# Kernel tuning notes

Measured on AMD Instinct MI355X. Metric: run time of the kernel, lower is better.

Reference implementation:

```python
import jax, jax.numpy as jnp
import numpy as np

B, N, A, M, H, KD, VD, O = 256, 2048, 256, 256, 8, 32, 32, 256
EPS = 1e-10

def setup_inputs() -> dict:
    key = jax.random.key(0)
    ks = jax.random.split(key, 8)
    return {
        "q_data": jax.random.normal(ks[0], (B, N, A), dtype=jnp.float32),
        "m_data": jax.random.normal(ks[1], (B, N, M), dtype=jnp.float32),
        "q_mask": jnp.ones((B, N, 1), dtype=jnp.float32),
        "bias": jnp.zeros((B, 1, N), dtype=jnp.float32),
        "query_w": 0.02 * jax.random.normal(ks[2], (A, H, KD), dtype=jnp.float32),
        "key_w": 0.02 * jax.random.normal(ks[3], (M, KD), dtype=jnp.float32),
        "value_w": 0.02 * jax.random.normal(ks[4], (M, VD), dtype=jnp.float32),
        "gating_w": 0.02 * jax.random.normal(ks[5], (A, H, VD), dtype=jnp.float32),
        "gating_b": jnp.zeros((H, VD), dtype=jnp.float32),
        "output_w": 0.02 * jax.random.normal(ks[6], (H, VD, O), dtype=jnp.float32),
        "output_b": jnp.zeros((O,), dtype=jnp.float32),
    }

def reference(q_data, m_data, q_mask, bias, query_w, key_w, value_w,
              gating_w, gating_b, output_w, output_b):
    # masked mean over the query axis: q_mask [B,N,1] broadcasts over channels
    q_avg = jnp.sum(q_mask * q_data, axis=1) / (jnp.sum(q_mask, axis=1) + EPS)  # [B,A]
    kd = query_w.shape[-1]
    q = jnp.einsum('ba,ahc->bhc', q_avg, query_w) * kd ** (-0.5)  # [B,H,KD]
    k = jnp.einsum('bka,ac->bkc', m_data, key_w)                  # [B,N,KD]
    v = jnp.einsum('bka,ac->bkc', m_data, value_w)                # [B,N,VD]
    # the incoming `bias` arg is overwritten by the module, as in the original
    attn_bias = 1e9 * (q_mask[:, None, :, 0] - 1.0)               # [B,1,N]
    logits = jnp.einsum('bhc,bkc->bhk', q, k) + attn_bias         # [B,H,N]
    weights = jax.nn.softmax(logits, axis=-1)
    weighted_avg = jnp.einsum('bhk,bkc->bhc', weights, v)         # [B,H,VD]
    # gating == True
    gate = jax.nn.sigmoid(jnp.einsum('bqc,chv->bqhv', q_data, gating_w) + gating_b)
    gated = weighted_avg[:, None] * gate                          # [B,N,H,VD]
    out = jnp.einsum('bqhc,hco->bqo', gated, output_w) + output_b # [B,N,O]
    return out
```

## Files before the change

### kernel.cpp

```cpp
#include <hip/hip_runtime.h>

#define B_ 256
#define N_ 2048
#define A_ 256
#define M_ 256
#define H_ 8
#define KD_ 32
#define VD_ 32
#define O_ 256

typedef float f32x4 __attribute__((ext_vector_type(4)));
typedef __bf16 bf16x8 __attribute__((ext_vector_type(8)));
typedef unsigned short u16x8 __attribute__((ext_vector_type(8)));

union FragU { u16x8 u; bf16x8 b; };

__device__ __forceinline__ unsigned short f2bf(float f) {
  union { __bf16 b; unsigned short u; } c;
  c.b = (__bf16)f;
  return c.u;
}
__device__ __forceinline__ float bf2f(unsigned short h) {
  return __uint_as_float(((unsigned int)h) << 16);
}

__device__ __forceinline__ void gll16(const void* gsrc, void* ldst) {
  __builtin_amdgcn_global_load_lds(
      (const __attribute__((address_space(1))) void*)gsrc,
      (__attribute__((address_space(3))) void*)ldst, 16, 0, 0);
}

__global__ void pack_weights(const float* __restrict__ gating_w,
                             const float* __restrict__ output_w,
                             const float* __restrict__ key_w,
                             const float* __restrict__ value_w,
                             unsigned short* __restrict__ wg,
                             unsigned short* __restrict__ wo,
                             unsigned short* __restrict__ wkv) {
  int idx = blockIdx.x * 256 + threadIdx.x;
  int j = idx & 7;
  int lane = (idx >> 3) & 63;
  int rest = idx >> 9;
  int kc = rest & 7, ct = rest >> 3;
  int row = kc * 32 + ((lane >> 4) << 3) + j;
  int col = ct * 16 + (lane & 15);
  wg[idx] = f2bf(gating_w[row * 256 + col]);
  wo[idx] = f2bf(output_w[row * 256 + col]);
  if (idx < 16384) {
    float v = (col < 32) ? key_w[row * 32 + col] : value_w[row * 32 + (col - 32)];
    wkv[idx] = f2bf(v);
  }
}

__global__ void reduce_q(const float* __restrict__ qd, const float* __restrict__ qm,
                         const float* __restrict__ qw, float* __restrict__ q_out) {
  int b = blockIdx.x;
  int t = threadIdx.x;
  int l = t & 63, g = t >> 6;
  const float* qdb = qd + (size_t)b * N_ * A_;
  const float* qmb = qm + (size_t)b * N_;
  f32x4 sum = {0.f, 0.f, 0.f, 0.f};
  float msum = 0.f;
  for (int n = g; n < N_; n += 16) {
    float m = qmb[n];
    msum += m;
    f32x4 v = *(const f32x4*)(qdb + (size_t)n * A_ + l * 4);
    sum += m * v;
  }
  __shared__ float s[16][256];
  __shared__ float ms[16];
  __shared__ float qavg[256];
  *(f32x4*)&s[g][l * 4] = sum;
  if (l == 0) ms[g] = msum;
  __syncthreads();
  if (t < 256) {
    float tot = 0.f;
#pragma unroll
    for (int k = 0; k < 16; k++) tot += s[k][t];
    float mt = 0.f;
#pragma unroll
    for (int k = 0; k < 16; k++) mt += ms[k];
    qavg[t] = tot / (mt + 1e-10f);
  }
  __syncthreads();
  if (t < 256) {
    float acc = 0.f;
    for (int a2 = 0; a2 < 256; a2++) acc += qavg[a2] * qw[a2 * 256 + t];
    q_out[b * 256 + t] = acc * 0.17677669529663687f;
  }
}

__global__ void kv_gemm(const float* __restrict__ md,
                        const unsigned short* __restrict__ wkv,
                        unsigned short* __restrict__ kv) {
  int t = threadIdx.x;
  int w = t >> 6, l = t & 63, q = l >> 4, l15 = l & 15;
  size_t r0 = (size_t)blockIdx.x * 128;
  f32x4 acc[2][4] = {};
  for (int kc = 0; kc < 8; kc++) {
    FragU bfr[4];
#pragma unroll
    for (int ct = 0; ct < 4; ct++)
      bfr[ct].u = *(const u16x8*)(wkv + (((ct * 8 + kc) * 64 + l) << 3));
    FragU af[2];
#pragma unroll
    for (int rt = 0; rt < 2; rt++) {
      size_t row = r0 + (size_t)(w * 32 + rt * 16 + l15);
      const float4* s4 = (const float4*)(md + row * 256 + kc * 32 + q * 8);
      float4 u0 = s4[0], u1 = s4[1];
      af[rt].u = (u16x8){f2bf(u0.x), f2bf(u0.y), f2bf(u0.z), f2bf(u0.w),
                         f2bf(u1.x), f2bf(u1.y), f2bf(u1.z), f2bf(u1.w)};
    }
#pragma unroll
    for (int ct = 0; ct < 4; ct++) {
      acc[0][ct] = __builtin_amdgcn_mfma_f32_16x16x32_bf16(af[0].b, bfr[ct].b, acc[0][ct], 0, 0, 0);
      acc[1][ct] = __builtin_amdgcn_mfma_f32_16x16x32_bf16(af[1].b, bfr[ct].b, acc[1][ct], 0, 0, 0);
    }
  }
#pragma unroll
  for (int rt = 0; rt < 2; rt++)
#pragma unroll
    for (int ct = 0; ct < 4; ct++)
#pragma unroll
      for (int r = 0; r < 4; r++) {
        size_t row = r0 + (size_t)(w * 32 + rt * 16 + q * 4 + r);
        kv[row * 64 + ct * 16 + l15] = f2bf(acc[rt][ct][r]);
      }
}

__global__ void attn_softmax(const unsigned short* __restrict__ kv,
                             const float* __restrict__ qv,
                             const float* __restrict__ qm,
                             float* __restrict__ wa) {
  int b = blockIdx.x, t = threadIdx.x;
  __shared__ float lg[8][2048];
  __shared__ float red[4][256];
  __shared__ float inv_s[8];
  const float* qb = qv + b * 256;
  const float* qmb = qm + (size_t)b * N_;
  for (int n = t; n < N_; n += 1024) {
    const u16x8* kr = (const u16x8*)(kv + ((size_t)(b * N_ + n)) * 64);
    float kf[32];
#pragma unroll
    for (int c8 = 0; c8 < 4; c8++) {
      u16x8 kk = kr[c8];
#pragma unroll
      for (int j = 0; j < 8; j++) kf[c8 * 8 + j] = bf2f(kk[j]);
    }
    float bias_n = 1e9f * (qmb[n] - 1.0f);
#pragma unroll
    for (int h = 0; h < 8; h++) {
      float d = 0.f;
#pragma unroll
      for (int c = 0; c < 32; c++) d += qb[h * 32 + c] * kf[c];
      lg[h][n] = d + bias_n;
    }
  }
  __syncthreads();
  if (t < 256) {
    int h = t >> 5, i = t & 31;
    float m = -3.0e38f;
    for (int n = i; n < N_; n += 32) m = fmaxf(m, lg[h][n]);
#pragma unroll
    for (int off = 16; off; off >>= 1) m = fmaxf(m, __shfl_xor(m, off));
    float s = 0.f;
    for (int n = i; n < N_; n += 32) {
      float e = __expf(lg[h][n] - m);
      lg[h][n] = e;
      s += e;
    }
#pragma unroll
    for (int off = 16; off; off >>= 1) s += __shfl_xor(s, off);
    if (i == 0) inv_s[h] = 1.0f / s;
  }
  __syncthreads();
  {
    int c = t & 31, h = (t >> 5) & 7, nq = t >> 8;
    const unsigned short* vb = kv + ((size_t)b * N_ + nq * 512) * 64 + 32 + c;
    const float* lgh = &lg[h][nq * 512];
    float acc = 0.f;
#pragma unroll 8
    for (int n = 0; n < 512; n++) acc += lgh[n] * bf2f(vb[(size_t)n * 64]);
    red[nq][t & 255] = acc;
  }
  __syncthreads();
  if (t < 256) {
    float r = red[0][t] + red[1][t] + red[2][t] + red[3][t];
    wa[b * 256 + t] = r * inv_s[t >> 5];
  }
}

__launch_bounds__(256)
__global__ void gate_out(const float* __restrict__ qd,
                         const unsigned short* __restrict__ wg,
                         const unsigned short* __restrict__ wo,
                         const float* __restrict__ wa,
                         const float* __restrict__ gb,
                         const float* __restrict__ ob,
                         float* __restrict__ out) {
  int blk = blockIdx.x;
  int b = blk >> 5, tile = blk & 31;
  int t = threadIdx.x;
  int w = t >> 6, l = t & 63, q = l >> 4, l15 = l & 15;
  __shared__ __attribute__((aligned(16))) unsigned short wst[2][16384];
  __shared__ __attribute__((aligned(16))) unsigned short Pt[4][16][40];
  __shared__ float wa_s[256], gb_s[256], ob_s[256];
  wa_s[t] = wa[b * 256 + t];
  gb_s[t] = gb[t];
  ob_s[t] = ob[t];
  size_t rowbase = (size_t)b * N_ + tile * 64;

  {
    const char* wgb = (const char*)wg;
    const char* wob = (const char*)wo;
    char* dst = (char*)&wst[0][0];
#pragma unroll
    for (int i = 0; i < 4; i++) {
      int ch = i * 4 + w;
      gll16(wgb + ch * 1024 + l * 16, dst + ch * 1024);
      gll16(wob + ch * 8192 + l * 16, dst + 16384 + ch * 1024);
    }
  }

  FragU af[8];
  {
    const float* src = qd + (rowbase + (size_t)(w * 16 + l15)) * 256 + q * 8;
#pragma unroll
    for (int kc = 0; kc < 8; kc++) {
      float4 u0 = *(const float4*)(src + kc * 32);
      float4 u1 = *(const float4*)(src + kc * 32 + 4);
      af[kc].u = (u16x8){f2bf(u0.x), f2bf(u0.y), f2bf(u0.z), f2bf(u0.w),
                         f2bf(u1.x), f2bf(u1.y), f2bf(u1.z), f2bf(u1.w)};
    }
  }
  f32x4 acc[16] = {};
  __syncthreads();

  for (int g = 0; g < 8; g++) {
    int cur = g & 1;
    if (g < 7) {
      const char* wgb = (const char*)wg + (size_t)(g + 1) * 16384;
      const char* wob = (const char*)wo + (size_t)(g + 1) * 1024;
      char* dst = (char*)&wst[cur ^ 1][0];
#pragma unroll
      for (int i = 0; i < 4; i++) {
        int ch = i * 4 + w;
        gll16(wgb + ch * 1024 + l * 16, dst + ch * 1024);
        gll16(wob + ch * 8192 + l * 16, dst + 16384 + ch * 1024);
      }
    }
    const unsigned short* wsl = &wst[cur][0];
    f32x4 gacc[2] = {};
#pragma unroll
    for (int kc = 0; kc < 8; kc++) {
      FragU b0, b1;
      b0.u = *(const u16x8*)(wsl + ((0 * 8 + kc) * 64 + l) * 8);
      b1.u = *(const u16x8*)(wsl + ((1 * 8 + kc) * 64 + l) * 8);
      gacc[0] = __builtin_amdgcn_mfma_f32_16x16x32_bf16(af[kc].b, b0.b, gacc[0], 0, 0, 0);
      gacc[1] = __builtin_amdgcn_mfma_f32_16x16x32_bf16(af[kc].b, b1.b, gacc[1], 0, 0, 0);
    }
#pragma unroll
    for (int ctl = 0; ctl < 2; ctl++) {
      int colg = ctl * 16 + l15;
      int col = g * 32 + colg;
      float wav = wa_s[col], gbv = gb_s[col];
#pragma unroll
      for (int r = 0; r < 4; r++) {
        float x = gacc[ctl][r] + gbv;
        float gate = 1.0f / (1.0f + __expf(-x));
        Pt[w][q * 4 + r][colg] = f2bf(wav * gate);
      }
    }
    FragU pf;
    pf.u = *(const u16x8*)&Pt[w][l15][q * 8];
#pragma unroll
    for (int ct = 0; ct < 16; ct++) {
      FragU bo;
      bo.u = *(const u16x8*)(wsl + 8192 + (ct * 64 + l) * 8);
      acc[ct] = __builtin_amdgcn_mfma_f32_16x16x32_bf16(pf.b, bo.b, acc[ct], 0, 0, 0);
    }
    __syncthreads();
  }
#pragma unroll
  for (int ct = 0; ct < 16; ct++) {
    int col = ct * 16 + l15;
    float obv = ob_s[col];
    size_t orow = (rowbase + (size_t)(w * 16 + q * 4)) * 256 + col;
#pragma unroll
    for (int r = 0; r < 4; r++)
      out[orow + (size_t)r * 256] = acc[ct][r] + obv;
  }
}

extern "C" void kernel_launch(void* const* d_in, const int* in_sizes, int n_in,
                              void* d_out, int out_size, void* d_ws, size_t ws_size,
                              hipStream_t stream) {
  const float* q_data   = (const float*)d_in[0];
  const float* m_data   = (const float*)d_in[1];
  const float* q_mask   = (const float*)d_in[2];
  const float* query_w  = (const float*)d_in[4];
  const float* key_w    = (const float*)d_in[5];
  const float* value_w  = (const float*)d_in[6];
  const float* gating_w = (const float*)d_in[7];
  const float* gating_b = (const float*)d_in[8];
  const float* output_w = (const float*)d_in[9];
  const float* output_b = (const float*)d_in[10];
  float* out = (float*)d_out;

  char* ws = (char*)d_ws;
  float* q_ws            = (float*)(ws);
  float* wa_ws           = (float*)(ws + (256 << 10));
  unsigned short* wg_ws  = (unsigned short*)(ws + (512 << 10));
  unsigned short* wo_ws  = (unsigned short*)(ws + (640 << 10));
  unsigned short* wkv_ws = (unsigned short*)(ws + (768 << 10));
  unsigned short* kv_ws  = (unsigned short*)(ws + (800 << 10));

  pack_weights<<<256, 256, 0, stream>>>(gating_w, output_w, key_w, value_w,
                                        wg_ws, wo_ws, wkv_ws);
  reduce_q<<<B_, 1024, 0, stream>>>(q_data, q_mask, query_w, q_ws);
  kv_gemm<<<(B_ * N_) / 128, 256, 0, stream>>>(m_data, wkv_ws, kv_ws);
  attn_softmax<<<B_, 1024, 0, stream>>>(kv_ws, q_ws, q_mask, wa_ws);
  gate_out<<<(B_ * N_) / 64, 256, 0, stream>>>(q_data, wg_ws, wo_ws, wa_ws,
                                               gating_b, output_b, out);
}
```

Before: 1.513 ms.

## Replace double-buffered weight staging with split single buffers to raise occupancy

Drops the double-buffered 64KB weight staging in gate_out in favour of two single 16KB buffers, one for gating weights and one for output weights. Each buffer's next slice is loaded right after its last use, with an extra barrier per iteration, so the gating-weight load overlaps the output MFMAs. Launch bounds now request 4 blocks per SM. The goal is higher occupancy to hide latency, at the cost of less prefetch distance and more synchronisation.

```diff
diff --git a/kernel.cpp b/kernel.cpp
--- a/kernel.cpp
+++ b/kernel.cpp
@@ -190,7 +190,7 @@
   }
 }
 
-__launch_bounds__(256)
+__launch_bounds__(256, 4)
 __global__ void gate_out(const float* __restrict__ qd,
                          const unsigned short* __restrict__ wg,
                          const unsigned short* __restrict__ wo,
@@ -202,7 +202,8 @@
   int b = blk >> 5, tile = blk & 31;
   int t = threadIdx.x;
   int w = t >> 6, l = t & 63, q = l >> 4, l15 = l & 15;
-  __shared__ __attribute__((aligned(16))) unsigned short wst[2][16384];
+  __shared__ __attribute__((aligned(16))) unsigned short wsg[8192];
+  __shared__ __attribute__((aligned(16))) unsigned short wso[8192];
   __shared__ __attribute__((aligned(16))) unsigned short Pt[4][16][40];
   __shared__ float wa_s[256], gb_s[256], ob_s[256];
   wa_s[t] = wa[b * 256 + t];
@@ -213,12 +214,11 @@
   {
     const char* wgb = (const char*)wg;
     const char* wob = (const char*)wo;
-    char* dst = (char*)&wst[0][0];
 #pragma unroll
     for (int i = 0; i < 4; i++) {
       int ch = i * 4 + w;
-      gll16(wgb + ch * 1024 + l * 16, dst + ch * 1024);
-      gll16(wob + ch * 8192 + l * 16, dst + 16384 + ch * 1024);
+      gll16(wgb + ch * 1024 + l * 16, (char*)wsg + ch * 1024);
+      gll16(wob + ch * 8192 + l * 16, (char*)wso + ch * 1024);
     }
   }
 
@@ -237,25 +237,12 @@
   __syncthreads();
 
   for (int g = 0; g < 8; g++) {
-    int cur = g & 1;
-    if (g < 7) {
-      const char* wgb = (const char*)wg + (size_t)(g + 1) * 16384;
-      const char* wob = (const char*)wo + (size_t)(g + 1) * 1024;
-      char* dst = (char*)&wst[cur ^ 1][0];
-#pragma unroll
-      for (int i = 0; i < 4; i++) {
-        int ch = i * 4 + w;
-        gll16(wgb + ch * 1024 + l * 16, dst + ch * 1024);
-        gll16(wob + ch * 8192 + l * 16, dst + 16384 + ch * 1024);
-      }
-    }
-    const unsigned short* wsl = &wst[cur][0];
     f32x4 gacc[2] = {};
 #pragma unroll
     for (int kc = 0; kc < 8; kc++) {
       FragU b0, b1;
-      b0.u = *(const u16x8*)(wsl + ((0 * 8 + kc) * 64 + l) * 8);
-      b1.u = *(const u16x8*)(wsl + ((1 * 8 + kc) * 64 + l) * 8);
+      b0.u = *(const u16x8*)(wsg + (kc * 64 + l) * 8);
+      b1.u = *(const u16x8*)(wsg + ((8 + kc) * 64 + l) * 8);
       gacc[0] = __builtin_amdgcn_mfma_f32_16x16x32_bf16(af[kc].b, b0.b, gacc[0], 0, 0, 0);
       gacc[1] = __builtin_amdgcn_mfma_f32_16x16x32_bf16(af[kc].b, b1.b, gacc[1], 0, 0, 0);
     }
@@ -273,13 +260,31 @@
     }
     FragU pf;
     pf.u = *(const u16x8*)&Pt[w][l15][q * 8];
+
+    __syncthreads();
+    if (g < 7) {
+      const char* wgb = (const char*)wg + (size_t)(g + 1) * 16384;
+#pragma unroll
+      for (int i = 0; i < 4; i++) {
+        int ch = i * 4 + w;
+        gll16(wgb + ch * 1024 + l * 16, (char*)wsg + ch * 1024);
+      }
+    }
 #pragma unroll
     for (int ct = 0; ct < 16; ct++) {
       FragU bo;
-      bo.u = *(const u16x8*)(wsl + 8192 + (ct * 64 + l) * 8);
+      bo.u = *(const u16x8*)(wso + (ct * 64 + l) * 8);
       acc[ct] = __builtin_amdgcn_mfma_f32_16x16x32_bf16(pf.b, bo.b, acc[ct], 0, 0, 0);
     }
     __syncthreads();
+    if (g < 7) {
+      const char* wob = (const char*)wo + (size_t)(g + 1) * 1024;
+#pragma unroll
+      for (int i = 0; i < 4; i++) {
+        int ch = i * 4 + w;
+        gll16(wob + ch * 8192 + l * 16, (char*)wso + ch * 1024);
+      }
+    }
   }
 #pragma unroll
   for (int ct = 0; ct < 16; ct++) {
```

After: 1.439 ms (median of 2 runs). -4.9%, faster.
